# Performance work log

Hardware: AMD Instinct MI355X
Metric: run time of the kernel (lower is better)

The kernel has to match this reference:

```python
import jax, jax.numpy as jnp
import numpy as np

N, E, ORDER, D, RANK = 4096, 16384, 3, 13, 128
NUM_PARAMS = ORDER + 1  # BT mode: ids = edge_types[:, i] in [0, order+1)
NUM_ITERS = 3
ATOMS = 7


def setup_inputs() -> dict:
    key = jax.random.key(0)
    ks = jax.random.split(key, 9)
    nodes = jax.random.normal(ks[0], (N, D), dtype=jnp.float32)
    edges = jax.random.randint(ks[1], (E, ORDER), 0, N)
    edge_types = jax.random.randint(ks[2], (E, ORDER), 0, NUM_PARAMS)
    atoms = jax.random.randint(ks[3], (E,), 0, ATOMS)
    atom_edges = jax.random.randint(ks[4], (E, ORDER), 0, ATOMS)
    # BPNet.params / bias: uniform(-1/sqrt(rank), 1/sqrt(rank))
    s1 = 1.0 / np.sqrt(RANK).astype(np.float32)
    bp_params = jax.random.uniform(ks[5], (NUM_PARAMS, D, RANK), minval=-s1, maxval=s1, dtype=jnp.float32)
    bp_bias = jax.random.uniform(ks[6], (NUM_PARAMS, 1, RANK), minval=-s1, maxval=s1, dtype=jnp.float32)
    # HighorderNet params per slot i: [NUM_PARAMS, hidden=RANK, out=D], uniform(-1/sqrt(D), 1/sqrt(D))
    s2 = 1.0 / np.sqrt(D).astype(np.float32)
    ho_params = jax.random.uniform(ks[7], (ORDER, NUM_PARAMS, RANK, D), minval=-s2, maxval=s2, dtype=jnp.float32)
    ho_bias = jax.random.uniform(ks[8], (ORDER, NUM_PARAMS, 1, D), minval=-s2, maxval=s2, dtype=jnp.float32)
    return {"nodes": nodes, "bp_params": bp_params, "bp_bias": bp_bias,
            "ho_params": ho_params, "ho_bias": ho_bias,
            "edges": edges, "edge_types": edge_types, "atoms": atoms, "atom_edges": atom_edges}


def _forward(nodes, bp_params, bp_bias, ho_params, ho_bias, edges, edge_types):
    n_nodes = nodes.shape[0]
    order = edges.shape[1]
    # Stage 1: per-slot gathered matmul rnodes @ W[edge_type] + b, then relu.
    rn = nodes[edges]                        # [E, order, D]
    W = bp_params[edge_types]                # [E, order, D, RANK]
    b = bp_bias[edge_types][:, :, 0, :]      # [E, order, RANK]
    t = jax.nn.relu(jnp.einsum('eod,eodr->eor', rn, W) + b)
    t = jnp.transpose(t, (1, 0, 2))          # [order, E, RANK]
    # Iterated message passing. NOTE: original loop re-reads the same
    # transform_cat each iteration (it is never updated), so every iteration
    # recomputes identical node_msg; we keep the loop for structural fidelity.
    node_msg = jnp.zeros((n_nodes, nodes.shape[1]), nodes.dtype)
    for _ in range(NUM_ITERS):
        node_msg = jnp.zeros((n_nodes, nodes.shape[1]), nodes.dtype)
        for i in range(order):
            # leave-one-out product over the other slots -> [E, RANK]
            others = [t[j] for j in range(order) if j != i]
            fact = others[0]
            for o in others[1:]:
                fact = fact * o
            Wi = ho_params[i][edge_types[:, i]]      # [E, RANK, D]
            bi = ho_bias[i][edge_types[:, i], 0]     # [E, D]
            msg = jnp.einsum('er,erd->ed', fact, Wi) + bi
            # dense one-hot incidence matmul == scatter-add over target nodes
            node_msg = node_msg + jax.ops.segment_sum(msg, edges[:, i], num_segments=n_nodes)
    return node_msg


def reference(nodes, bp_params, bp_bias, ho_params, ho_bias, edges, edge_types, atoms, atom_edges):
    # atoms / atom_edges unused in 'BT' mode (kept for signature fidelity)
    return _forward(nodes, bp_params, bp_bias, ho_params, ho_bias, edges, edge_types)
```

## Files before the change

kernel.cpp:

```cpp
#include <hip/hip_runtime.h>


#define DD 13
#define OD 3
#define NP 4
#define RK 128

typedef unsigned int uint;
typedef _Float16 h2 __attribute__((ext_vector_type(2)));

#define W2H_OFF 0
#define W2H_N   (12 * 13 * 64)
#define W1H_OFF (W2H_OFF + W2H_N)
#define W1H_N   (4 * 7 * 128)
#define B1F_OFF (W1H_OFF + W1H_N)
#define B1F_N   (4 * 128)
#define HOB_OFF (B1F_OFF + B1F_N)
#define HOB_N   (12 * 16)
#define TAB_N   (HOB_OFF + HOB_N)
#define NROW_OFF TAB_N
#define NROW_N  (8 * 12 * 8)
#define SH_N    (TAB_N + NROW_N)

__device__ __forceinline__ uint pk(float lo, float hi) {
    return __builtin_bit_cast(uint, __builtin_amdgcn_cvt_pkrtz(lo, hi));
}
__device__ __forceinline__ h2 ash2(uint w) { return __builtin_bit_cast(h2, w); }

template <int CTRL>
__device__ __forceinline__ float dpp_add(float x) {
    int p = __builtin_amdgcn_update_dpp(0, __float_as_int(x), CTRL, 0xF, 0xF, false);
    return x + __int_as_float(p);
}
__device__ __forceinline__ float row_sum16(float x) {
    x = dpp_add<0xB1>(x);
    x = dpp_add<0x4E>(x);
    x = dpp_add<0x141>(x);
    x = dpp_add<0x140>(x);
    return x;
}

__global__ __launch_bounds__(256) void bpnet_pack(
    const float* __restrict__ bp_params,
    const float* __restrict__ bp_bias,
    const float* __restrict__ ho_params,
    const float* __restrict__ ho_bias,
    uint* __restrict__ ws)
{
    const int tid = blockIdx.x * 256 + threadIdx.x;
    if (tid < W1H_OFF) {
        const int c = tid & 63, q = tid >> 6;
        const int dd = q % 13, it = q / 13;
        ws[tid] = pk(ho_params[(size_t)(it * RK + 2 * c) * DD + dd],
                     ho_params[(size_t)(it * RK + 2 * c + 1) * DD + dd]);
    } else if (tid < B1F_OFF) {
        const int j = tid - W1H_OFF;
        const int r = j & 127, q = j >> 7;
        const int p = q % 7, ty = q / 7;
        const float a = bp_params[(ty * DD + 2 * p) * RK + r];
        const float b = (2 * p + 1 < DD) ? bp_params[(ty * DD + 2 * p + 1) * RK + r] : 0.f;
        ws[tid] = pk(a, b);
    } else if (tid < HOB_OFF) {
        ((float*)ws)[tid] = bp_bias[tid - B1F_OFF];
    } else if (tid < TAB_N) {
        const int j = tid - HOB_OFF;
        const int dd = j & 15, it = j >> 4;
        ((float*)ws)[tid] = (dd < DD) ? ho_bias[it * DD + dd] : 0.f;
    }
}

__global__ __launch_bounds__(512, 4) void bpnet_fused(
    const float* __restrict__ nodes,
    const int*   __restrict__ edges,
    const int*   __restrict__ edge_types,
    const uint*  __restrict__ tab,
    float*       __restrict__ out)
{
    __shared__ __align__(16) uint sh[SH_N];
    const int tid = threadIdx.x;

    for (int k4 = tid; k4 < TAB_N / 4; k4 += 512)
        ((uint4*)sh)[k4] = ((const uint4*)tab)[k4];
    __syncthreads();

    const int lane = tid & 63;
    const int wv   = tid >> 6;
    const int e4   = lane >> 4;
    const int g    = lane & 15;
    const int eb   = (blockIdx.x * 8 + wv) * 4;

    int ev = 0, tv = 0;
    if (lane < 12) {
        ev = edges[eb * OD + lane];
        tv = edge_types[eb * OD + lane];
    }

    uint* mynr = sh + NROW_OFF + wv * 96;
#pragma unroll
    for (int pass = 0; pass < 2; ++pass) {
        const int idx = pass * 64 + lane;
        if (idx < 96) {
            const int r = idx >> 3, p = idx & 7;
            const int nr_ = __shfl(ev, r, 64);
            uint v = 0;
            if (p < 6)       v = pk(nodes[(size_t)nr_ * DD + 2 * p],
                                    nodes[(size_t)nr_ * DD + 2 * p + 1]);
            else if (p == 6) v = pk(nodes[(size_t)nr_ * DD + 12], 0.f);
            mynr[r * 8 + p] = v;
        }
    }

    int tg[OD], et[OD];
#pragma unroll
    for (int i = 0; i < OD; ++i) {
        tg[i] = __shfl(ev, e4 * OD + i, 64);
        et[i] = __shfl(tv, e4 * OD + i, 64);
    }

    float t[OD][8];
#pragma unroll
    for (int o = 0; o < OD; ++o) {
        const uint* nh = mynr + (e4 * OD + o) * 8;
        const uint4 n0 = *(const uint4*)(nh);
        const uint4 n1 = *(const uint4*)(nh + 4);
        const float* bf = (const float*)(sh + B1F_OFF) + et[o] * RK + 8 * g;
        const float4 b0 = *(const float4*)(bf);
        const float4 b1 = *(const float4*)(bf + 4);
        float s[8] = {b0.x, b0.y, b0.z, b0.w, b1.x, b1.y, b1.z, b1.w};
        const uint* wb = sh + W1H_OFF + (et[o] * 7) * RK + 8 * g;
#define S1(p, nv) { const uint4 wA = *(const uint4*)(wb + (p) * RK);          \
                    const uint4 wB = *(const uint4*)(wb + (p) * RK + 4);      \
            const h2 nn = ash2(nv);                                           \
            s[0] = __builtin_amdgcn_fdot2(nn, ash2(wA.x), s[0], false);       \
            s[1] = __builtin_amdgcn_fdot2(nn, ash2(wA.y), s[1], false);       \
            s[2] = __builtin_amdgcn_fdot2(nn, ash2(wA.z), s[2], false);       \
            s[3] = __builtin_amdgcn_fdot2(nn, ash2(wA.w), s[3], false);       \
            s[4] = __builtin_amdgcn_fdot2(nn, ash2(wB.x), s[4], false);       \
            s[5] = __builtin_amdgcn_fdot2(nn, ash2(wB.y), s[5], false);       \
            s[6] = __builtin_amdgcn_fdot2(nn, ash2(wB.z), s[6], false);       \
            s[7] = __builtin_amdgcn_fdot2(nn, ash2(wB.w), s[7], false); }
        S1(0, n0.x) S1(1, n0.y) S1(2, n0.z) S1(3, n0.w)
        S1(4, n1.x) S1(5, n1.y) S1(6, n1.z)
#undef S1
#pragma unroll
        for (int r = 0; r < 8; ++r) t[o][r] = fmaxf(s[r], 0.f);
    }

#pragma unroll
    for (int i = 0; i < OD; ++i) {
        const int j = (i + 1) % OD, k = (i + 2) % OD;
        uint fh[4];
#pragma unroll
        for (int r = 0; r < 4; ++r)
            fh[r] = pk(t[j][2 * r] * t[k][2 * r], t[j][2 * r + 1] * t[k][2 * r + 1]);
        const int it = i * NP + et[i];
        const uint* wb = sh + W2H_OFF + (it * DD) * 64 + 4 * g;
        float c[DD];
#pragma unroll
        for (int dd = 0; dd < DD; ++dd) {
            const uint4 w = *(const uint4*)(wb + dd * 64);
            float a = __builtin_amdgcn_fdot2(ash2(fh[0]), ash2(w.x), 0.f, false);
            a = __builtin_amdgcn_fdot2(ash2(fh[1]), ash2(w.y), a, false);
            a = __builtin_amdgcn_fdot2(ash2(fh[2]), ash2(w.z), a, false);
            a = __builtin_amdgcn_fdot2(ash2(fh[3]), ash2(w.w), a, false);
            c[dd] = a;
        }
#pragma unroll
        for (int dd = 0; dd < DD; ++dd) c[dd] = row_sum16(c[dd]);
        float q = c[0];
#pragma unroll
        for (int dd = 1; dd < DD; ++dd) q = (g == dd) ? c[dd] : q;
        q += ((const float*)(sh + HOB_OFF))[it * 16 + g];
        if (g < DD) atomicAdd(out + (size_t)tg[i] * DD + g, q);
    }
}

extern "C" void kernel_launch(void* const* d_in, const int* in_sizes, int n_in,
                              void* d_out, int out_size, void* d_ws, size_t ws_size,
                              hipStream_t stream) {
    const float* nodes      = (const float*)d_in[0];
    const float* bp_params  = (const float*)d_in[1];
    const float* bp_bias    = (const float*)d_in[2];
    const float* ho_params  = (const float*)d_in[3];
    const float* ho_bias    = (const float*)d_in[4];
    const int*   edges      = (const int*)d_in[5];
    const int*   edge_types = (const int*)d_in[6];
    float* out = (float*)d_out;
    uint*  ws  = (uint*)d_ws;

    const int E = in_sizes[5] / OD;

    (void)hipMemsetAsync(out, 0, (size_t)out_size * sizeof(float), stream);

    bpnet_pack<<<(TAB_N + 255) / 256, 256, 0, stream>>>(
        bp_params, bp_bias, ho_params, ho_bias, ws);

    bpnet_fused<<<E / 32, 512, 0, stream>>>(nodes, edges, edge_types, ws, out);
}
```

Measured before the change: 82.87 us.

## Fold output zeroing into pack kernel, split W1 layout, overlap table load

Removes the separate memset by zeroing the output inside the pack kernel, which saves one launch. Splits the stage-1 weight and bias tables into two 64-wide halves so each lane reads contiguous 16-byte chunks with a stride that is intended to avoid LDS bank conflicts. Moves the shared-memory table copy after the node gather so the two global loads can overlap. The pack grid is small, so zeroing the output in it relies on a grid-stride loop over few threads.

```diff
diff --git a/kernel.cpp b/kernel.cpp
--- a/kernel.cpp
+++ b/kernel.cpp
@@ -11,11 +11,15 @@
 
 #define W2H_OFF 0
 #define W2H_N   (12 * 13 * 64)
-#define W1H_OFF (W2H_OFF + W2H_N)
-#define W1H_N   (4 * 7 * 128)
-#define B1F_OFF (W1H_OFF + W1H_N)
-#define B1F_N   (4 * 128)
-#define HOB_OFF (B1F_OFF + B1F_N)
+#define W1A_OFF (W2H_OFF + W2H_N)
+#define W1A_N   (4 * 7 * 64)
+#define W1B_OFF (W1A_OFF + W1A_N)
+#define W1B_N   (4 * 7 * 64)
+#define B1A_OFF (W1B_OFF + W1B_N)
+#define B1A_N   (4 * 64)
+#define B1B_OFF (B1A_OFF + B1A_N)
+#define B1B_N   (4 * 64)
+#define HOB_OFF (B1B_OFF + B1B_N)
 #define HOB_N   (12 * 16)
 #define TAB_N   (HOB_OFF + HOB_N)
 #define NROW_OFF TAB_N
@@ -45,23 +49,45 @@
     const float* __restrict__ bp_bias,
     const float* __restrict__ ho_params,
     const float* __restrict__ ho_bias,
-    uint* __restrict__ ws)
+    uint* __restrict__ ws,
+    uint* __restrict__ outz, int out_n)
 {
     const int tid = blockIdx.x * 256 + threadIdx.x;
-    if (tid < W1H_OFF) {
+    const int nthr = gridDim.x * 256;
+
+    const int n4 = out_n >> 2;
+    for (int k = tid; k < n4; k += nthr) ((uint4*)outz)[k] = uint4{0, 0, 0, 0};
+    if (tid < (out_n & 3)) outz[(n4 << 2) + tid] = 0;
+
+    if (tid < W1A_OFF) {
         const int c = tid & 63, q = tid >> 6;
         const int dd = q % 13, it = q / 13;
         ws[tid] = pk(ho_params[(size_t)(it * RK + 2 * c) * DD + dd],
                      ho_params[(size_t)(it * RK + 2 * c + 1) * DD + dd]);
-    } else if (tid < B1F_OFF) {
-        const int j = tid - W1H_OFF;
-        const int r = j & 127, q = j >> 7;
+    } else if (tid < W1B_OFF) {
+        const int j = tid - W1A_OFF;
+        const int c = j & 63, q = j >> 6;
         const int p = q % 7, ty = q / 7;
+        const int r = 8 * (c >> 2) + (c & 3);
         const float a = bp_params[(ty * DD + 2 * p) * RK + r];
         const float b = (2 * p + 1 < DD) ? bp_params[(ty * DD + 2 * p + 1) * RK + r] : 0.f;
         ws[tid] = pk(a, b);
+    } else if (tid < B1A_OFF) {
+        const int j = tid - W1B_OFF;
+        const int c = j & 63, q = j >> 6;
+        const int p = q % 7, ty = q / 7;
+        const int r = 8 * (c >> 2) + 4 + (c & 3);
+        const float a = bp_params[(ty * DD + 2 * p) * RK + r];
+        const float b = (2 * p + 1 < DD) ? bp_params[(ty * DD + 2 * p + 1) * RK + r] : 0.f;
+        ws[tid] = pk(a, b);
+    } else if (tid < B1B_OFF) {
+        const int j = tid - B1A_OFF;
+        const int c = j & 63, ty = j >> 6;
+        ((float*)ws)[tid] = bp_bias[ty * RK + 8 * (c >> 2) + (c & 3)];
     } else if (tid < HOB_OFF) {
-        ((float*)ws)[tid] = bp_bias[tid - B1F_OFF];
+        const int j = tid - B1B_OFF;
+        const int c = j & 63, ty = j >> 6;
+        ((float*)ws)[tid] = bp_bias[ty * RK + 8 * (c >> 2) + 4 + (c & 3)];
     } else if (tid < TAB_N) {
         const int j = tid - HOB_OFF;
         const int dd = j & 15, it = j >> 4;
@@ -77,12 +103,7 @@
     float*       __restrict__ out)
 {
     __shared__ __align__(16) uint sh[SH_N];
-    const int tid = threadIdx.x;
-
-    for (int k4 = tid; k4 < TAB_N / 4; k4 += 512)
-        ((uint4*)sh)[k4] = ((const uint4*)tab)[k4];
-    __syncthreads();
-
+    const int tid  = threadIdx.x;
     const int lane = tid & 63;
     const int wv   = tid >> 6;
     const int e4   = lane >> 4;
@@ -110,6 +131,10 @@
         }
     }
 
+    for (int k4 = tid; k4 < TAB_N / 4; k4 += 512)
+        ((uint4*)sh)[k4] = ((const uint4*)tab)[k4];
+    __syncthreads();
+
     int tg[OD], et[OD];
 #pragma unroll
     for (int i = 0; i < OD; ++i) {
@@ -123,13 +148,13 @@
         const uint* nh = mynr + (e4 * OD + o) * 8;
         const uint4 n0 = *(const uint4*)(nh);
         const uint4 n1 = *(const uint4*)(nh + 4);
-        const float* bf = (const float*)(sh + B1F_OFF) + et[o] * RK + 8 * g;
-        const float4 b0 = *(const float4*)(bf);
-        const float4 b1 = *(const float4*)(bf + 4);
+        const float4 b0 = *(const float4*)((const float*)(sh + B1A_OFF) + et[o] * 64 + 4 * g);
+        const float4 b1 = *(const float4*)((const float*)(sh + B1B_OFF) + et[o] * 64 + 4 * g);
         float s[8] = {b0.x, b0.y, b0.z, b0.w, b1.x, b1.y, b1.z, b1.w};
-        const uint* wb = sh + W1H_OFF + (et[o] * 7) * RK + 8 * g;
-#define S1(p, nv) { const uint4 wA = *(const uint4*)(wb + (p) * RK);          \
-                    const uint4 wB = *(const uint4*)(wb + (p) * RK + 4);      \
+        const uint* wa = sh + W1A_OFF + (et[o] * 7) * 64 + 4 * g;
+        const uint* wb = sh + W1B_OFF + (et[o] * 7) * 64 + 4 * g;
+#define S1(p, nv) { const uint4 wA = *(const uint4*)(wa + (p) * 64);          \
+                    const uint4 wB = *(const uint4*)(wb + (p) * 64);          \
             const h2 nn = ash2(nv);                                           \
             s[0] = __builtin_amdgcn_fdot2(nn, ash2(wA.x), s[0], false);       \
             s[1] = __builtin_amdgcn_fdot2(nn, ash2(wA.y), s[1], false);       \
@@ -154,11 +179,11 @@
         for (int r = 0; r < 4; ++r)
             fh[r] = pk(t[j][2 * r] * t[k][2 * r], t[j][2 * r + 1] * t[k][2 * r + 1]);
         const int it = i * NP + et[i];
-        const uint* wb = sh + W2H_OFF + (it * DD) * 64 + 4 * g;
+        const uint* wb2 = sh + W2H_OFF + (it * DD) * 64 + 4 * g;
         float c[DD];
 #pragma unroll
         for (int dd = 0; dd < DD; ++dd) {
-            const uint4 w = *(const uint4*)(wb + dd * 64);
+            const uint4 w = *(const uint4*)(wb2 + dd * 64);
             float a = __builtin_amdgcn_fdot2(ash2(fh[0]), ash2(w.x), 0.f, false);
             a = __builtin_amdgcn_fdot2(ash2(fh[1]), ash2(w.y), a, false);
             a = __builtin_amdgcn_fdot2(ash2(fh[2]), ash2(w.z), a, false);
@@ -190,10 +215,8 @@
 
     const int E = in_sizes[5] / OD;
 
-    (void)hipMemsetAsync(out, 0, (size_t)out_size * sizeof(float), stream);
-
     bpnet_pack<<<(TAB_N + 255) / 256, 256, 0, stream>>>(
-        bp_params, bp_bias, ho_params, ho_bias, ws);
+        bp_params, bp_bias, ho_params, ho_bias, ws, (uint*)out, out_size);
 
     bpnet_fused<<<E / 32, 512, 0, stream>>>(nodes, edges, edge_types, ws, out);
 }
```

After: 80.58 us, median of 2. -2.8%, faster.

## Precompute per-(node,type) stage-1 activations in prep kernel and gather them

Applied to the files above, without the earlier changes.

Stage 1 (relu(node @ W[type] + b)) depends only on the node and the edge type. A prep kernel now computes it once for every (node, type) pair, 4096×4 entries of 128 fp16 values, and the fused kernel gathers these rows instead of recomputing the matmul for each edge slot. The prep kernel also zeroes the output and packs the second-stage weights, which replaces the separate memset and pack launches. The fused kernel issues its activation gathers before the shared-memory table copy so the two overlap. The slot products are now done in fp16 instead of fp32, which slightly changes precision.

```diff
diff --git a/kernel.cpp b/kernel.cpp
--- a/kernel.cpp
+++ b/kernel.cpp
@@ -11,21 +11,21 @@
 
 #define W2H_OFF 0
 #define W2H_N   (12 * 13 * 64)
-#define W1H_OFF (W2H_OFF + W2H_N)
-#define W1H_N   (4 * 7 * 128)
-#define B1F_OFF (W1H_OFF + W1H_N)
-#define B1F_N   (4 * 128)
-#define HOB_OFF (B1F_OFF + B1F_N)
+#define HOB_OFF (W2H_OFF + W2H_N)
 #define HOB_N   (12 * 16)
 #define TAB_N   (HOB_OFF + HOB_N)
-#define NROW_OFF TAB_N
-#define NROW_N  (8 * 12 * 8)
-#define SH_N    (TAB_N + NROW_N)
+#define T_OFF   16384
+#define T_N     (16384 * 64)
+
+#define ZERO_N4 13312
+#define AUX_N   (ZERO_N4 + W2H_N + HOB_N)
+#define TBLK    4096
 
 __device__ __forceinline__ uint pk(float lo, float hi) {
     return __builtin_bit_cast(uint, __builtin_amdgcn_cvt_pkrtz(lo, hi));
 }
 __device__ __forceinline__ h2 ash2(uint w) { return __builtin_bit_cast(h2, w); }
+__device__ __forceinline__ uint asu(h2 v) { return __builtin_bit_cast(uint, v); }
 
 template <int CTRL>
 __device__ __forceinline__ float dpp_add(float x) {
@@ -40,49 +40,60 @@
     return x;
 }
 
-__global__ __launch_bounds__(256) void bpnet_pack(
+__global__ __launch_bounds__(256) void bpnet_prep(
+    const float* __restrict__ nodes,
     const float* __restrict__ bp_params,
     const float* __restrict__ bp_bias,
     const float* __restrict__ ho_params,
     const float* __restrict__ ho_bias,
-    uint* __restrict__ ws)
+    uint* __restrict__ ws,
+    uint* __restrict__ outz)
 {
-    const int tid = blockIdx.x * 256 + threadIdx.x;
-    if (tid < W1H_OFF) {
-        const int c = tid & 63, q = tid >> 6;
-        const int dd = q % 13, it = q / 13;
-        ws[tid] = pk(ho_params[(size_t)(it * RK + 2 * c) * DD + dd],
-                     ho_params[(size_t)(it * RK + 2 * c + 1) * DD + dd]);
-    } else if (tid < B1F_OFF) {
-        const int j = tid - W1H_OFF;
-        const int r = j & 127, q = j >> 7;
-        const int p = q % 7, ty = q / 7;
-        const float a = bp_params[(ty * DD + 2 * p) * RK + r];
-        const float b = (2 * p + 1 < DD) ? bp_params[(ty * DD + 2 * p + 1) * RK + r] : 0.f;
-        ws[tid] = pk(a, b);
-    } else if (tid < HOB_OFF) {
-        ((float*)ws)[tid] = bp_bias[tid - B1F_OFF];
-    } else if (tid < TAB_N) {
-        const int j = tid - HOB_OFF;
-        const int dd = j & 15, it = j >> 4;
-        ((float*)ws)[tid] = (dd < DD) ? ho_bias[it * DD + dd] : 0.f;
+    const int thr = threadIdx.x;
+    if (blockIdx.x < TBLK) {
+        const int c    = thr & 63;
+        const int pair = blockIdx.x * 4 + (thr >> 6);
+        const int ty   = pair & 3, node = pair >> 2;
+        const float* nr = nodes + (size_t)node * DD;
+        float nv[DD];
+#pragma unroll
+        for (int d = 0; d < DD; ++d) nv[d] = nr[d];
+        const float* wp = bp_params + (ty * DD) * RK + 2 * c;
+        float lo = bp_bias[ty * RK + 2 * c];
+        float hi = bp_bias[ty * RK + 2 * c + 1];
+#pragma unroll
+        for (int d = 0; d < DD; ++d) {
+            const float2 w = *(const float2*)(wp + d * RK);
+            lo = fmaf(nv[d], w.x, lo);
+            hi = fmaf(nv[d], w.y, hi);
+        }
+        ws[T_OFF + pair * 64 + c] = pk(fmaxf(lo, 0.f), fmaxf(hi, 0.f));
+    } else {
+        const int j = (blockIdx.x - TBLK) * 256 + thr;
+        if (j < ZERO_N4) {
+            ((uint4*)outz)[j] = uint4{0, 0, 0, 0};
+        } else if (j < ZERO_N4 + W2H_N) {
+            const int idx = j - ZERO_N4;
+            const int c = idx & 63, q = idx >> 6;
+            const int dd = q % 13, it = q / 13;
+            ws[W2H_OFF + idx] = pk(ho_params[(size_t)(it * RK + 2 * c) * DD + dd],
+                                   ho_params[(size_t)(it * RK + 2 * c + 1) * DD + dd]);
+        } else if (j < AUX_N) {
+            const int jj = j - (ZERO_N4 + W2H_N);
+            const int dd = jj & 15, it = jj >> 4;
+            ((float*)ws)[HOB_OFF + jj] = (dd < DD) ? ho_bias[it * DD + dd] : 0.f;
+        }
     }
 }
 
 __global__ __launch_bounds__(512, 4) void bpnet_fused(
-    const float* __restrict__ nodes,
     const int*   __restrict__ edges,
     const int*   __restrict__ edge_types,
-    const uint*  __restrict__ tab,
+    const uint*  __restrict__ ws,
     float*       __restrict__ out)
 {
-    __shared__ __align__(16) uint sh[SH_N];
-    const int tid = threadIdx.x;
-
-    for (int k4 = tid; k4 < TAB_N / 4; k4 += 512)
-        ((uint4*)sh)[k4] = ((const uint4*)tab)[k4];
-    __syncthreads();
-
+    __shared__ __align__(16) uint sh[TAB_N];
+    const int tid  = threadIdx.x;
     const int lane = tid & 63;
     const int wv   = tid >> 6;
     const int e4   = lane >> 4;
@@ -94,22 +105,6 @@
         ev = edges[eb * OD + lane];
         tv = edge_types[eb * OD + lane];
     }
-
-    uint* mynr = sh + NROW_OFF + wv * 96;
-#pragma unroll
-    for (int pass = 0; pass < 2; ++pass) {
-        const int idx = pass * 64 + lane;
-        if (idx < 96) {
-            const int r = idx >> 3, p = idx & 7;
-            const int nr_ = __shfl(ev, r, 64);
-            uint v = 0;
-            if (p < 6)       v = pk(nodes[(size_t)nr_ * DD + 2 * p],
-                                    nodes[(size_t)nr_ * DD + 2 * p + 1]);
-            else if (p == 6) v = pk(nodes[(size_t)nr_ * DD + 12], 0.f);
-            mynr[r * 8 + p] = v;
-        }
-    }
-
     int tg[OD], et[OD];
 #pragma unroll
     for (int i = 0; i < OD; ++i) {
@@ -117,48 +112,29 @@
         et[i] = __shfl(tv, e4 * OD + i, 64);
     }
 
-    float t[OD][8];
+    uint4 th[OD];
 #pragma unroll
-    for (int o = 0; o < OD; ++o) {
-        const uint* nh = mynr + (e4 * OD + o) * 8;
-        const uint4 n0 = *(const uint4*)(nh);
-        const uint4 n1 = *(const uint4*)(nh + 4);
-        const float* bf = (const float*)(sh + B1F_OFF) + et[o] * RK + 8 * g;
-        const float4 b0 = *(const float4*)(bf);
-        const float4 b1 = *(const float4*)(bf + 4);
-        float s[8] = {b0.x, b0.y, b0.z, b0.w, b1.x, b1.y, b1.z, b1.w};
-        const uint* wb = sh + W1H_OFF + (et[o] * 7) * RK + 8 * g;
-#define S1(p, nv) { const uint4 wA = *(const uint4*)(wb + (p) * RK);          \
-                    const uint4 wB = *(const uint4*)(wb + (p) * RK + 4);      \
-            const h2 nn = ash2(nv);                                           \
-            s[0] = __builtin_amdgcn_fdot2(nn, ash2(wA.x), s[0], false);       \
-            s[1] = __builtin_amdgcn_fdot2(nn, ash2(wA.y), s[1], false);       \
-            s[2] = __builtin_amdgcn_fdot2(nn, ash2(wA.z), s[2], false);       \
-            s[3] = __builtin_amdgcn_fdot2(nn, ash2(wA.w), s[3], false);       \
-            s[4] = __builtin_amdgcn_fdot2(nn, ash2(wB.x), s[4], false);       \
-            s[5] = __builtin_amdgcn_fdot2(nn, ash2(wB.y), s[5], false);       \
-            s[6] = __builtin_amdgcn_fdot2(nn, ash2(wB.z), s[6], false);       \
-            s[7] = __builtin_amdgcn_fdot2(nn, ash2(wB.w), s[7], false); }
-        S1(0, n0.x) S1(1, n0.y) S1(2, n0.z) S1(3, n0.w)
-        S1(4, n1.x) S1(5, n1.y) S1(6, n1.z)
-#undef S1
-#pragma unroll
-        for (int r = 0; r < 8; ++r) t[o][r] = fmaxf(s[r], 0.f);
-    }
+    for (int o = 0; o < OD; ++o)
+        th[o] = *(const uint4*)(ws + T_OFF + (tg[o] * NP + et[o]) * 64 + 4 * g);
+
+    for (int k4 = tid; k4 < TAB_N / 4; k4 += 512)
+        ((uint4*)sh)[k4] = ((const uint4*)ws)[k4];
+    __syncthreads();
 
 #pragma unroll
     for (int i = 0; i < OD; ++i) {
         const int j = (i + 1) % OD, k = (i + 2) % OD;
         uint fh[4];
-#pragma unroll
-        for (int r = 0; r < 4; ++r)
-            fh[r] = pk(t[j][2 * r] * t[k][2 * r], t[j][2 * r + 1] * t[k][2 * r + 1]);
+        fh[0] = asu(ash2(th[j].x) * ash2(th[k].x));
+        fh[1] = asu(ash2(th[j].y) * ash2(th[k].y));
+        fh[2] = asu(ash2(th[j].z) * ash2(th[k].z));
+        fh[3] = asu(ash2(th[j].w) * ash2(th[k].w));
         const int it = i * NP + et[i];
-        const uint* wb = sh + W2H_OFF + (it * DD) * 64 + 4 * g;
+        const uint* wb2 = sh + W2H_OFF + (it * DD) * 64 + 4 * g;
         float c[DD];
 #pragma unroll
         for (int dd = 0; dd < DD; ++dd) {
-            const uint4 w = *(const uint4*)(wb + dd * 64);
+            const uint4 w = *(const uint4*)(wb2 + dd * 64);
             float a = __builtin_amdgcn_fdot2(ash2(fh[0]), ash2(w.x), 0.f, false);
             a = __builtin_amdgcn_fdot2(ash2(fh[1]), ash2(w.y), a, false);
             a = __builtin_amdgcn_fdot2(ash2(fh[2]), ash2(w.z), a, false);
@@ -190,10 +166,9 @@
 
     const int E = in_sizes[5] / OD;
 
-    (void)hipMemsetAsync(out, 0, (size_t)out_size * sizeof(float), stream);
+    const int aux_blocks = (AUX_N + 255) / 256;
+    bpnet_prep<<<TBLK + aux_blocks, 256, 0, stream>>>(
+        nodes, bp_params, bp_bias, ho_params, ho_bias, ws, (uint*)out);
 
-    bpnet_pack<<<(TAB_N + 255) / 256, 256, 0, stream>>>(
-        bp_params, bp_bias, ho_params, ho_bias, ws);
-
-    bpnet_fused<<<E / 32, 512, 0, stream>>>(nodes, edges, edge_types, ws, out);
+    bpnet_fused<<<E / 32, 512, 0, stream>>>(edges, edge_types, ws, out);
 }
```

Measured after the change: 88.21 us. +6.4%, slower.
